# Optimization experiments

Measured on AMD Instinct MI355X. Metric: run time of the kernel, lower is better.

Reference implementation:

```python
import jax, jax.numpy as jnp
import numpy as np

EPS_LN = 1e-5
EPS_BN = 1e-5


def ln_channels(x, w, b):
    # LayerNorm2d: normalize over channel dim of NCHW
    mu = x.mean(axis=1, keepdims=True)
    var = x.var(axis=1, keepdims=True)
    return (x - mu) / jnp.sqrt(var + EPS_LN) * w[None, :, None, None] + b[None, :, None, None]


def bn_eval(x, g, b):
    # eval-mode BatchNorm2d with running_mean=0, running_var=1
    return x / jnp.sqrt(1.0 + EPS_BN) * g[None, :, None, None] + b[None, :, None, None]


def conv1x1(x, w, b):
    return jnp.einsum('bchw,oc->bohw', x, w) + b[None, :, None, None]


def q_shift(x):
    # directional shift: 4 channel quarters shifted right/left/down/up by 1 px (zero pad)
    C = x.shape[1]
    q = C // 4
    return jnp.concatenate([
        jnp.pad(x[:, 0 * q:1 * q, :, :-1], ((0, 0), (0, 0), (0, 0), (1, 0))),
        jnp.pad(x[:, 1 * q:2 * q, :, 1:], ((0, 0), (0, 0), (0, 0), (0, 1))),
        jnp.pad(x[:, 2 * q:3 * q, :-1, :], ((0, 0), (0, 0), (1, 0), (0, 0))),
        jnp.pad(x[:, 3 * q:4 * q, 1:, :], ((0, 0), (0, 0), (0, 1), (0, 0))),
    ], axis=1)


def wkv_scan(k, v, w_neg, u):
    # numerically-stable RWKV WKV recurrence. k, v: [N, T, C]; w_neg (negative decay), u: [C]
    N, T, C = k.shape

    def step(carry, kv):
        a, b, p = carry
        kt, vt = kv
        q = jnp.maximum(p, u + kt)
        e1 = jnp.exp(p - q)
        e2 = jnp.exp(u + kt - q)
        out = (e1 * a + e2 * vt) / (e1 * b + e2)
        q2 = jnp.maximum(p + w_neg, kt)
        f1 = jnp.exp(p + w_neg - q2)
        f2 = jnp.exp(kt - q2)
        return (f1 * a + f2 * vt, f1 * b + f2, q2), out

    init = (jnp.zeros((N, C), k.dtype), jnp.zeros((N, C), k.dtype), jnp.full((N, C), -1e38, k.dtype))
    _, outs = jax.lax.scan(step, init, (jnp.swapaxes(k, 0, 1), jnp.swapaxes(v, 0, 1)))
    return jnp.swapaxes(outs, 0, 1)


def shape_guided_rwkv(x, mask, mix_k, mix_v, mix_r, Wk, Wv, Wr, Wo, decay, first, kn_w, kn_b):
    B, C, H, W = x.shape
    xs = q_shift(x)
    x_sh = mask * xs + (1.0 - mask) * x  # saliency-guided shift blend
    mk = mix_k[None, :, None, None]
    mv = mix_v[None, :, None, None]
    mr = mix_r[None, :, None, None]
    xk = x * mk + x_sh * (1.0 - mk)
    xv = x * mv + x_sh * (1.0 - mv)
    xr = x * mr + x_sh * (1.0 - mr)
    k = jnp.einsum('bchw,oc->bohw', xk, Wk)
    v = jnp.einsum('bchw,oc->bohw', xv, Wv)
    sr = jax.nn.sigmoid(jnp.einsum('bchw,oc->bohw', xr, Wr))
    w_neg = -jnp.exp(decay)
    # horizontal orientation: scan each row left->right
    kh = k.transpose(0, 2, 3, 1).reshape(B * H, W, C)
    vh = v.transpose(0, 2, 3, 1).reshape(B * H, W, C)
    wkv_h = wkv_scan(kh, vh, w_neg, first).reshape(B, H, W, C).transpose(0, 3, 1, 2)
    # vertical orientation: scan each column top->bottom
    kv_ = k.transpose(0, 3, 2, 1).reshape(B * W, H, C)
    vv_ = v.transpose(0, 3, 2, 1).reshape(B * W, H, C)
    wkv_v = wkv_scan(kv_, vv_, w_neg, first).reshape(B, W, H, C).transpose(0, 3, 2, 1)
    wkv = 0.5 * (wkv_h + wkv_v)
    wkv = ln_channels(wkv, kn_w, kn_b)  # key_norm=True
    out = jnp.einsum('bchw,oc->bohw', sr * wkv, Wo)
    return x + out


def channel_fusion(x, c1_w, c1_b, bn1_g, bn1_b, c2_w, c2_b, bn2_g, bn2_b, c3_w, c3_b, bn3_g, bn3_b):
    # grouped 3x3 conv (groups=2) -> GELU -> BN -> 1x1 expand -> GELU -> BN -> 1x1 reduce -> GELU -> BN
    y = jax.lax.conv_general_dilated(x, c1_w, (1, 1), 'SAME',
                                     dimension_numbers=('NCHW', 'OIHW', 'NCHW'),
                                     feature_group_count=2) + c1_b[None, :, None, None]
    y = bn_eval(jax.nn.gelu(y, approximate=False), bn1_g, bn1_b)
    y = bn_eval(jax.nn.gelu(conv1x1(y, c2_w, c2_b), approximate=False), bn2_g, bn2_b)
    y = bn_eval(jax.nn.gelu(conv1x1(y, c3_w, c3_b), approximate=False), bn3_g, bn3_b)
    return y


def patch_expand(x, up_w, up_b, s=2):
    B, C, H, W = x.shape
    y = conv1x1(x, up_w, up_b)  # [B, Cout*s*s, H, W]
    Cout = y.shape[1] // (s * s)
    y = y.reshape(B, Cout, s, s, H, W).transpose(0, 1, 4, 2, 5, 3).reshape(B, Cout, H * s, W * s)
    return y


def setup_inputs() -> dict:
    key = jax.random.key(0)
    B, C, Cs, Cout, H, W, s = 8, 256, 512, 128, 64, 64, 2
    ks = jax.random.split(key, 32)
    sc = C ** -0.5
    inp = {
        'x': jax.random.normal(ks[0], (B, C, H, W), jnp.float32),
        'skip': jax.random.normal(ks[1], (B, Cs, H, W), jnp.float32),
        'saliency_mask': jax.random.uniform(ks[2], (B, 1, H, W), jnp.float32),
        'ln1_w': jnp.ones((C,)), 'ln1_b': jnp.zeros((C,)),
        'ln2_w': jnp.ones((C,)), 'ln2_b': jnp.zeros((C,)),
        'mix_k': jax.random.uniform(ks[3], (C,)),
        'mix_v': jax.random.uniform(ks[4], (C,)),
        'mix_r': jax.random.uniform(ks[5], (C,)),
        'Wk': jax.random.normal(ks[6], (C, C)) * sc,
        'Wv': jax.random.normal(ks[7], (C, C)) * sc,
        'Wr': jax.random.normal(ks[8], (C, C)) * sc,
        'Wo': jax.random.normal(ks[9], (C, C)) * sc,
        'decay': jax.random.normal(ks[10], (C,)) * 0.5,
        'first': jax.random.normal(ks[11], (C,)) * 0.5,
        'kn_w': jnp.ones((C,)), 'kn_b': jnp.zeros((C,)),
        'sp_w': jax.random.normal(ks[12], (C, Cs)) * (Cs ** -0.5),
        'sp_b': jnp.zeros((C,)),
        'c1_w': jax.random.normal(ks[13], (2 * C, C, 3, 3)) * ((C * 9) ** -0.5),
        'c1_b': jnp.zeros((2 * C,)),
        'bn1_g': jnp.ones((2 * C,)), 'bn1_b': jnp.zeros((2 * C,)),
        'c2_w': jax.random.normal(ks[14], (4 * C, 2 * C)) * ((2 * C) ** -0.5),
        'c2_b': jnp.zeros((4 * C,)),
        'bn2_g': jnp.ones((4 * C,)), 'bn2_b': jnp.zeros((4 * C,)),
        'c3_w': jax.random.normal(ks[15], (C, 4 * C)) * ((4 * C) ** -0.5),
        'c3_b': jnp.zeros((C,)),
        'bn3_g': jnp.ones((C,)), 'bn3_b': jnp.zeros((C,)),
        'up_w': jax.random.normal(ks[16], (Cout * s * s, C)) * sc,
        'up_b': jnp.zeros((Cout * s * s,)),
    }
    return inp


def reference(x, skip, saliency_mask, ln1_w, ln1_b, ln2_w, ln2_b, mix_k, mix_v, mix_r,
              Wk, Wv, Wr, Wo, decay, first, kn_w, kn_b, sp_w, sp_b,
              c1_w, c1_b, bn1_g, bn1_b, c2_w, c2_b, bn2_g, bn2_b, c3_w, c3_b, bn3_g, bn3_b,
              up_w, up_b):
    xn = ln_channels(x, ln1_w, ln1_b)
    x_sg = shape_guided_rwkv(xn, saliency_mask, mix_k, mix_v, mix_r, Wk, Wv, Wr, Wo,
                             decay, first, kn_w, kn_b)
    skip_feat = conv1x1(skip, sp_w, sp_b)
    x_cat = jnp.concatenate([x_sg, skip_feat], axis=1)
    x_fused = channel_fusion(x_cat, c1_w, c1_b, bn1_g, bn1_b, c2_w, c2_b, bn2_g, bn2_b,
                             c3_w, c3_b, bn3_g, bn3_b)
    x_fused = ln_channels(x_fused, ln2_w, ln2_b)
    return patch_expand(x_fused, up_w, up_b, s=2)
```

## Files before the change

### kernel.cpp

```cpp
#include <hip/hip_runtime.h>
#include <hip/hip_bf16.h>
#include <math.h>

#define B_ 8
#define C_ 256
#define P_ 4096

typedef __bf16 bf16_t;
typedef __attribute__((ext_vector_type(8))) __bf16 bf16x8;
typedef __attribute__((ext_vector_type(4))) float f32x4;

template<typename T>
__global__ __launch_bounds__(256)
void ln_stats_kernel(const T* __restrict__ in, float2* __restrict__ stats)
{
    __shared__ float sred[4][64];
    __shared__ float s2red[4][64];
    int tid = threadIdx.x;
    int wp = tid & 63, cw = tid >> 6;
    int gp = blockIdx.x * 64 + wp;
    int b  = gp >> 12, p = gp & 4095;
    size_t base = (size_t)b * 256 * 4096 + p;
    float s = 0.f, s2 = 0.f;
    #pragma unroll 8
    for (int cc = 0; cc < 64; ++cc) {
        float v = (float)in[base + (size_t)(cw * 64 + cc) * 4096];
        s += v; s2 += v * v;
    }
    sred[cw][wp] = s; s2red[cw][wp] = s2;
    __syncthreads();
    if (cw == 0) {
        s  = sred[0][wp]  + sred[1][wp]  + sred[2][wp]  + sred[3][wp];
        s2 = s2red[0][wp] + s2red[1][wp] + s2red[2][wp] + s2red[3][wp];
        float mu  = s * (1.f / 256.f);
        float var = s2 * (1.f / 256.f) - mu * mu;
        stats[gp] = make_float2(mu, 1.0f / sqrtf(var + 1e-5f));
    }
}

__global__ __launch_bounds__(256)
void qshift_mix_kernel(const float* __restrict__ x, const float2* __restrict__ st1,
                       const float* __restrict__ mask,
                       const float* __restrict__ gw, const float* __restrict__ gb,
                       const float* __restrict__ mk_, const float* __restrict__ mv_,
                       const float* __restrict__ mr_,
                       bf16_t* __restrict__ xk, bf16_t* __restrict__ xv,
                       bf16_t* __restrict__ xr)
{
    int g = blockIdx.x * 256 + threadIdx.x;
    int p = g & 4095;
    int c = (g >> 12) & 255;
    int b = g >> 20;
    int h = p >> 6, w = p & 63;
    float gwc = gw[c], gbc = gb[c];
    float2 stc = st1[(b << 12) + p];
    float xcv = (x[g] - stc.x) * stc.y * gwc + gbc;
    float xs = 0.f;
    int quad = c >> 6;
    int d = 0; bool ok = false;
    if (quad == 0)      { ok = (w > 0);  d = -1;  }
    else if (quad == 1) { ok = (w < 63); d = 1;   }
    else if (quad == 2) { ok = (h > 0);  d = -64; }
    else                { ok = (h < 63); d = 64;  }
    if (ok) {
        float2 st2 = st1[(b << 12) + p + d];
        xs = (x[g + d] - st2.x) * st2.y * gwc + gbc;
    }
    float m = mask[(b << 12) + p];
    float xsh = m * xs + (1.f - m) * xcv;
    float a;
    a = mk_[c]; xk[g] = (bf16_t)(a * xcv + (1.f - a) * xsh);
    a = mv_[c]; xv[g] = (bf16_t)(a * xcv + (1.f - a) * xsh);
    a = mr_[c]; xr[g] = (bf16_t)(a * xcv + (1.f - a) * xsh);
}

#define EP_NONE    0
#define EP_SIGMOID 1
#define EP_BIAS    2
#define EP_RESLN   3
#define EP_GELU_BN 4
#define EP_SHUFFLE 5
#define EP_KVR     6

template<int NB, int BMODE, int EPI, int OUTBF>
__global__ __launch_bounds__(256, 2)
void mfma_gemm(const bf16_t* __restrict__ Wp, const void* __restrict__ Xin,
               const bf16_t* __restrict__ X2,
               const float2* __restrict__ bstats, const float* __restrict__ blnw,
               const float* __restrict__ blnb,
               const float* __restrict__ bias, const float* __restrict__ bng,
               const float* __restrict__ bnb,
               const float* __restrict__ resx, const float2* __restrict__ estats,
               const float* __restrict__ elnw, const float* __restrict__ elnb,
               void* __restrict__ OutV,
               int O, int K, int Cstride, int obs, int ocoff)
{
    constexpr int BROWS = (NB == 3) ? 2 * 66 : 128;
    __shared__ bf16_t Alds[NB * 128 * 36];
    __shared__ bf16_t Blds[BROWS * 36];
    int tid = threadIdx.x;
    int bx = blockIdx.x;
    int o0 = blockIdx.y * 128;
    int b  = blockIdx.z;
    int p0 = bx << 7;
    int cbase = (NB == 3) ? ((o0 >> 8) << 8) : 0;

    const bf16_t* Wpe = (EPI == EP_KVR) ? Wp + (size_t)(b >> 3) * O * K : Wp;

    int lane = tid & 63, wid = tid >> 6;
    int l15 = lane & 15;
    int lk8 = (lane >> 4) << 3;
    int mbase = (wid >> 1) << 6;
    int nbase = (wid & 1) << 6;

    const bf16_t* Xb_bf = (const bf16_t*)Xin + (size_t)b * Cstride * 4096;
    const float*  Xb_f  = (const float*)Xin + (size_t)b * Cstride * 4096;
    const bf16_t* X2b   = (BMODE == 3) ? X2 + (size_t)b * Cstride * 4096 : nullptr;

    f32x4 acc[4][4] = {};

    if (NB == 3 && tid < 144) {
        int r = tid / 72, rest = tid % 72;
        int col = rest / 36, cc = rest % 36;
        Blds[(r * 66 + (col ? 65 : 0)) * 36 + cc] = (bf16_t)0.f;
    }

    for (int kh = 0; kh < NB; ++kh) {
        for (int c0 = 0; c0 < K; c0 += 32) {
            __syncthreads();
            if (NB == 3) {
                int wpos = tid & 63, cgr = tid >> 6;
                #pragma unroll
                for (int r = 0; r < 2; ++r) {
                    int hr = (bx << 1) + kh - 1 + r;
                    bf16x8 bv;
                    #pragma unroll
                    for (int i = 0; i < 8; ++i) bv[i] = (bf16_t)0.f;
                    if (hr >= 0 && hr < 64) {
                        size_t gb = (size_t)(cbase + c0 + cgr * 8) * 4096 + (hr << 6) + wpos;
                        #pragma unroll
                        for (int j = 0; j < 8; ++j) bv[j] = Xb_bf[gb + (size_t)j * 4096];
                    }
                    *reinterpret_cast<bf16x8*>(&Blds[(r * 66 + wpos + 1) * 36 + cgr * 8]) = bv;
                }
            } else {
                #pragma unroll
                for (int rep = 0; rep < 2; ++rep) {
                    int p_loc = tid & 127;
                    int cgr = (tid >> 7) + rep * 2;
                    bf16x8 bv;
                    size_t gbase = (size_t)(c0 + cgr * 8) * 4096 + p0 + p_loc;
                    float2 st = make_float2(0.f, 1.f);
                    if (BMODE >= 2) st = bstats[(b << 12) + p0 + p_loc];
                    #pragma unroll
                    for (int j = 0; j < 8; ++j) {
                        size_t gi = gbase + (size_t)j * 4096;
                        int cc = c0 + cgr * 8 + j;
                        if (BMODE == 0)      bv[j] = Xb_bf[gi];
                        else if (BMODE == 1) bv[j] = (bf16_t)Xb_f[gi];
                        else {
                            float v = ((float)Xb_bf[gi] - st.x) * st.y * blnw[cc] + blnb[cc];
                            if (BMODE == 3) v *= (float)X2b[gi];
                            bv[j] = (bf16_t)v;
                        }
                    }
                    *reinterpret_cast<bf16x8*>(&Blds[p_loc * 36 + cgr * 8]) = bv;
                }
            }
            {
                int ao = tid >> 1, aq = tid & 1;
                #pragma unroll
                for (int t = 0; t < NB; ++t) {
                    const bf16_t* wsrc = (NB == 3)
                        ? Wpe + ((size_t)(kh * 3 + t) * O + o0 + ao) * 256 + c0
                        : Wpe + (size_t)(o0 + ao) * K + c0;
                    bf16x8 w0 = *reinterpret_cast<const bf16x8*>(wsrc + aq * 8);
                    bf16x8 w1 = *reinterpret_cast<const bf16x8*>(wsrc + (aq + 2) * 8);
                    *reinterpret_cast<bf16x8*>(&Alds[(t * 128 + ao) * 36 + aq * 8]) = w0;
                    *reinterpret_cast<bf16x8*>(&Alds[(t * 128 + ao) * 36 + (aq + 2) * 8]) = w1;
                }
            }
            __syncthreads();
            #pragma unroll
            for (int t = 0; t < NB; ++t) {
                bf16x8 af[4];
                #pragma unroll
                for (int i = 0; i < 4; ++i)
                    af[i] = *reinterpret_cast<const bf16x8*>(
                              &Alds[(t * 128 + mbase + i * 16 + l15) * 36 + lk8]);
                #pragma unroll
                for (int j = 0; j < 4; ++j) {
                    int pl = nbase + j * 16;
                    int baddr;
                    if (NB == 3)
                        baddr = ((pl >> 6) * 66 + (pl & 63) + l15 + t) * 36 + lk8;
                    else
                        baddr = (pl + l15) * 36 + lk8;
                    bf16x8 bfv = *reinterpret_cast<const bf16x8*>(&Blds[baddr]);
                    #pragma unroll
                    for (int i = 0; i < 4; ++i)
                        acc[i][j] = __builtin_amdgcn_mfma_f32_16x16x32_bf16(
                                        af[i], bfv, acc[i][j], 0, 0, 0);
                }
            }
        }
    }

    const float bnsc = 1.0f / sqrtf(1.f + 1e-5f);
    bool kvr_sig = (EPI == EP_KVR) && (b >= 16);
    #pragma unroll
    for (int i = 0; i < 4; ++i) {
        #pragma unroll
        for (int r = 0; r < 4; ++r) {
            int o = o0 + mbase + i * 16 + ((lane >> 4) << 2) + r;
            float bi = (EPI == EP_BIAS || EPI == EP_GELU_BN || EPI == EP_SHUFFLE)
                       ? bias[o] : 0.f;
            float sc = 0.f, sh = 0.f;
            if (EPI == EP_GELU_BN) { sc = bng[o] * bnsc; sh = bnb[o]; }
            float rw = 0.f, rb = 0.f;
            if (EPI == EP_RESLN) { rw = elnw[o]; rb = elnb[o]; }
            #pragma unroll
            for (int j = 0; j < 4; ++j) {
                int pp = p0 + nbase + j * 16 + l15;
                float t = acc[i][j][r];
                if (EPI == EP_SIGMOID) t = 1.f / (1.f + expf(-t));
                if (EPI == EP_KVR && kvr_sig) t = 1.f / (1.f + expf(-t));
                if (EPI == EP_BIAS || EPI == EP_GELU_BN || EPI == EP_SHUFFLE) t += bi;
                if (EPI == EP_RESLN) {
                    float2 st = estats[(b << 12) + pp];
                    float rv = resx[((size_t)b * 256 + o) * 4096 + pp];
                    t += (rv - st.x) * st.y * rw + rb;
                }
                if (EPI == EP_GELU_BN) {
                    t = 0.5f * t * (1.f + erff(t * 0.70710678118654752f));
                    t = t * sc + sh;
                }
                if (EPI == EP_SHUFFLE) {
                    int co = o >> 2, s1 = (o >> 1) & 1, s2 = o & 1;
                    int hh = pp >> 6, ww = pp & 63;
                    ((float*)OutV)[(((size_t)b * 128 + co) * 128 + hh * 2 + s1) * 128
                                   + ww * 2 + s2] = t;
                } else {
                    size_t oidx = ((size_t)b * obs + ocoff + o) * 4096 + pp;
                    if (OUTBF) ((bf16_t*)OutV)[oidx] = (bf16_t)t;
                    else       ((float*)OutV)[oidx]  = t;
                }
            }
        }
    }
}

__global__ __launch_bounds__(256)
void pack_all_kernel(const float* __restrict__ wk, const float* __restrict__ wv,
                     const float* __restrict__ wr, const float* __restrict__ wo,
                     const float* __restrict__ sp, const float* __restrict__ c2,
                     const float* __restrict__ c3, const float* __restrict__ up,
                     const float* __restrict__ c1, bf16_t* __restrict__ outfl,
                     bf16_t* __restrict__ outc1)
{
    int g = blockIdx.x * 256 + threadIdx.x;
    if (g < 1310720) {
        float v;
        if      (g < 65536)   v = wk[g];
        else if (g < 131072)  v = wv[g - 65536];
        else if (g < 196608)  v = wr[g - 131072];
        else if (g < 262144)  v = wo[g - 196608];
        else if (g < 393216)  v = sp[g - 262144];
        else if (g < 917504)  v = c2[g - 393216];
        else if (g < 1179648) v = c3[g - 917504];
        else                  v = up[g - 1179648];
        outfl[g] = (bf16_t)v;
    } else {
        int g2 = g - 1310720;
        if (g2 < 1179648) {
            int c = g2 & 255;
            int o = (g2 >> 8) & 511;
            int tap = g2 >> 17;
            outc1[g2] = (bf16_t)c1[(size_t)o * 2304 + c * 9 + tap];
        }
    }
}

__global__ __launch_bounds__(64)
void wkv_h_kernel(const bf16_t* __restrict__ kin, const bf16_t* __restrict__ vin,
                  bf16_t* __restrict__ outw,
                  const float* __restrict__ decay, const float* __restrict__ first)
{
    __shared__ bf16_t ks[64 * 66];
    __shared__ bf16_t vs[64 * 66];
    int c0 = blockIdx.x * 64;
    int h  = blockIdx.y;
    int b  = blockIdx.z;
    int tid = threadIdx.x;
    size_t base = (((size_t)b * 256 + c0) * 64 + h) * 64;

    for (int f = tid; f < 64 * 64; f += 64) {
        int cc = f >> 6, w = f & 63;
        ks[cc * 66 + w] = kin[base + (size_t)cc * 4096 + w];
        vs[cc * 66 + w] = vin[base + (size_t)cc * 4096 + w];
    }
    __syncthreads();

    int c = c0 + tid;
    float u  = first[c];
    float wn = -expf(decay[c]);
    float a = 0.f, bb = 0.f, pp = -1e38f;
    for (int t = 0; t < 64; ++t) {
        float kt = (float)ks[tid * 66 + t], vt = (float)vs[tid * 66 + t];
        float q  = fmaxf(pp, u + kt);
        float e1 = expf(pp - q), e2 = expf(u + kt - q);
        float ov = (e1 * a + e2 * vt) / (e1 * bb + e2);
        ks[tid * 66 + t] = (bf16_t)ov;
        float q2 = fmaxf(pp + wn, kt);
        float f1 = expf(pp + wn - q2), f2 = expf(kt - q2);
        a = f1 * a + f2 * vt;
        bb = f1 * bb + f2;
        pp = q2;
    }
    __syncthreads();
    for (int f = tid; f < 64 * 64; f += 64) {
        int cc = f >> 6, w = f & 63;
        outw[base + (size_t)cc * 4096 + w] = ks[cc * 66 + w];
    }
}

__global__ __launch_bounds__(256)
void wkv_v_kernel(const bf16_t* __restrict__ kin, const bf16_t* __restrict__ vin,
                  bf16_t* __restrict__ outw,
                  const float* __restrict__ decay, const float* __restrict__ first)
{
    int g = blockIdx.x * 256 + threadIdx.x;
    int w = g & 63;
    int c = (g >> 6) & 255;
    int b = g >> 14;
    size_t base = (size_t)(b * 256 + c) * 4096 + w;
    float u  = first[c];
    float wn = -expf(decay[c]);
    float a = 0.f, bb = 0.f, pp = -1e38f;
    for (int h = 0; h < 64; ++h) {
        size_t idx = base + h * 64;
        float kt = (float)kin[idx], vt = (float)vin[idx];
        float q  = fmaxf(pp, u + kt);
        float e1 = expf(pp - q), e2 = expf(u + kt - q);
        float ov = (e1 * a + e2 * vt) / (e1 * bb + e2);
        outw[idx] = (bf16_t)(0.5f * ((float)outw[idx] + ov));
        float q2 = fmaxf(pp + wn, kt);
        float f1 = expf(pp + wn - q2), f2 = expf(kt - q2);
        a = f1 * a + f2 * vt;
        bb = f1 * bb + f2;
        pp = q2;
    }
}

extern "C" void kernel_launch(void* const* d_in, const int* in_sizes, int n_in,
                              void* d_out, int out_size, void* d_ws, size_t ws_size,
                              hipStream_t stream)
{
    const float* x      = (const float*)d_in[0];
    const float* skip   = (const float*)d_in[1];
    const float* mask   = (const float*)d_in[2];
    const float* ln1_w  = (const float*)d_in[3];
    const float* ln1_b  = (const float*)d_in[4];
    const float* ln2_w  = (const float*)d_in[5];
    const float* ln2_b  = (const float*)d_in[6];
    const float* mix_k  = (const float*)d_in[7];
    const float* mix_v  = (const float*)d_in[8];
    const float* mix_r  = (const float*)d_in[9];
    const float* Wk     = (const float*)d_in[10];
    const float* Wv     = (const float*)d_in[11];
    const float* Wr     = (const float*)d_in[12];
    const float* Wo     = (const float*)d_in[13];
    const float* decay  = (const float*)d_in[14];
    const float* first  = (const float*)d_in[15];
    const float* kn_w   = (const float*)d_in[16];
    const float* kn_b   = (const float*)d_in[17];
    const float* sp_w   = (const float*)d_in[18];
    const float* sp_b   = (const float*)d_in[19];
    const float* c1_w   = (const float*)d_in[20];
    const float* c1_b   = (const float*)d_in[21];
    const float* bn1_g  = (const float*)d_in[22];
    const float* bn1_b  = (const float*)d_in[23];
    const float* c2_w   = (const float*)d_in[24];
    const float* c2_b   = (const float*)d_in[25];
    const float* bn2_g  = (const float*)d_in[26];
    const float* bn2_b  = (const float*)d_in[27];
    const float* c3_w   = (const float*)d_in[28];
    const float* c3_b   = (const float*)d_in[29];
    const float* bn3_g  = (const float*)d_in[30];
    const float* bn3_b  = (const float*)d_in[31];
    const float* up_w   = (const float*)d_in[32];
    const float* up_b   = (const float*)d_in[33];
    float* out = (float*)d_out;

    float* ws = (float*)d_ws;
    const size_t S = 8388608;
    const size_t Hs = S / 2;
    bf16_t* xk   = (bf16_t*)ws;
    bf16_t* xv   = (bf16_t*)(ws + Hs);
    bf16_t* xr   = (bf16_t*)(ws + 2 * Hs);
    bf16_t* kbuf = (bf16_t*)(ws + 3 * Hs);
    bf16_t* vbuf = (bf16_t*)(ws + 4 * Hs);
    bf16_t* rbuf = (bf16_t*)(ws + 5 * Hs);
    bf16_t* wkv  = (bf16_t*)(ws + 6 * Hs);
    bf16_t* xcat = (bf16_t*)(ws + 7 * Hs);
    bf16_t* y1   = (bf16_t*)(ws + 9 * Hs);
    bf16_t* y2   = (bf16_t*)ws;
    bf16_t* y3   = (bf16_t*)(ws + 4 * Hs);
    float*  wtop = ws + 11 * Hs;
    bf16_t* w9   = (bf16_t*)wtop;
    bf16_t* wfl  = w9 + 1179648;
    float2* st1  = (float2*)(wfl + 1310720);
    float2* stk  = st1 + 32768;
    float2* st2  = stk + 32768;
    bf16_t* wkb = wfl;
    bf16_t* wob = wfl + 196608;
    bf16_t* spb = wfl + 262144;
    bf16_t* c2b = wfl + 393216;
    bf16_t* c3b = wfl + 917504;
    bf16_t* upb = wfl + 1179648;

    dim3 blk(256);

    pack_all_kernel<<<dim3(9728), blk, 0, stream>>>(Wk, Wv, Wr, Wo, sp_w, c2_w,
                                                    c3_w, up_w, c1_w, wfl, w9);
    ln_stats_kernel<float><<<dim3(512), blk, 0, stream>>>(x, st1);

    qshift_mix_kernel<<<dim3(32768), blk, 0, stream>>>(x, st1, mask, ln1_w, ln1_b,
                                                       mix_k, mix_v, mix_r, xk, xv, xr);
    mfma_gemm<1, 0, EP_KVR, 1><<<dim3(32, 2, 24), blk, 0, stream>>>(
        wkb, xk, nullptr, nullptr, nullptr, nullptr, nullptr, nullptr, nullptr,
        nullptr, nullptr, nullptr, nullptr, kbuf, 256, 256, 256, 256, 0);
    wkv_h_kernel<<<dim3(4, 64, 8), dim3(64), 0, stream>>>(kbuf, vbuf, wkv, decay, first);
    wkv_v_kernel<<<dim3(512), blk, 0, stream>>>(kbuf, vbuf, wkv, decay, first);
    ln_stats_kernel<bf16_t><<<dim3(512), blk, 0, stream>>>(wkv, stk);
    mfma_gemm<1, 3, EP_RESLN, 1><<<dim3(32, 2, 8), blk, 0, stream>>>(
        wob, wkv, rbuf, stk, kn_w, kn_b, nullptr, nullptr, nullptr,
        x, st1, ln1_w, ln1_b, xcat, 256, 256, 256, 512, 0);
    mfma_gemm<1, 1, EP_BIAS, 1><<<dim3(32, 2, 8), blk, 0, stream>>>(
        spb, skip, nullptr, nullptr, nullptr, nullptr, sp_b, nullptr, nullptr,
        nullptr, nullptr, nullptr, nullptr, xcat, 256, 512, 512, 512, 256);
    mfma_gemm<3, 0, EP_GELU_BN, 1><<<dim3(32, 4, 8), blk, 0, stream>>>(
        w9, xcat, nullptr, nullptr, nullptr, nullptr, c1_b, bn1_g, bn1_b,
        nullptr, nullptr, nullptr, nullptr, y1, 512, 256, 512, 512, 0);
    mfma_gemm<1, 0, EP_GELU_BN, 1><<<dim3(32, 8, 8), blk, 0, stream>>>(
        c2b, y1, nullptr, nullptr, nullptr, nullptr, c2_b, bn2_g, bn2_b,
        nullptr, nullptr, nullptr, nullptr, y2, 1024, 512, 512, 1024, 0);
    mfma_gemm<1, 0, EP_GELU_BN, 1><<<dim3(32, 2, 8), blk, 0, stream>>>(
        c3b, y2, nullptr, nullptr, nullptr, nullptr, c3_b, bn3_g, bn3_b,
        nullptr, nullptr, nullptr, nullptr, y3, 256, 1024, 1024, 256, 0);
    ln_stats_kernel<bf16_t><<<dim3(512), blk, 0, stream>>>(y3, st2);
    mfma_gemm<1, 2, EP_SHUFFLE, 0><<<dim3(32, 4, 8), blk, 0, stream>>>(
        upb, y3, nullptr, st2, ln2_w, ln2_b, up_b, nullptr, nullptr,
        nullptr, nullptr, nullptr, nullptr, out, 512, 256, 256, 0, 0);
}
```

Measured before the change: 531.0 us.

## Load GEMM weight tiles directly into LDS with swizzled layout

Replaces the register-staged weight tile copy in the MFMA GEMM with global_load_lds direct-to-LDS transfers into an unpadded 32-wide row layout. To avoid LDS bank conflicts without padding, weights are pre-swizzled during packing with an XOR pattern on 8-element column groups, and the fragment reads apply the matching swizzle. This saves VGPR traffic and LDS footprint, but it couples the pack kernel layout to the GEMM read pattern and depends on the swizzle being consistent for every weight matrix.

```diff
diff --git a/kernel.cpp b/kernel.cpp
--- a/kernel.cpp
+++ b/kernel.cpp
@@ -9,6 +9,12 @@
 typedef __bf16 bf16_t;
 typedef __attribute__((ext_vector_type(8))) __bf16 bf16x8;
 typedef __attribute__((ext_vector_type(4))) float f32x4;
+
+__device__ __forceinline__ int swzc(int o, int c)
+{
+    int f = (o & 3) ^ ((o >> 2) & 3);
+    return (c & ~31) | ((((c >> 3) & 3) ^ f) << 3) | (c & 7);
+}
 
 template<typename T>
 __global__ __launch_bounds__(256)
@@ -96,7 +102,7 @@
                int O, int K, int Cstride, int obs, int ocoff)
 {
     constexpr int BROWS = (NB == 3) ? 2 * 66 : 128;
-    __shared__ bf16_t Alds[NB * 128 * 36];
+    __shared__ bf16_t Alds[NB * 128 * 32];
     __shared__ bf16_t Blds[BROWS * 36];
     int tid = threadIdx.x;
     int bx = blockIdx.x;
@@ -109,9 +115,11 @@
 
     int lane = tid & 63, wid = tid >> 6;
     int l15 = lane & 15;
-    int lk8 = (lane >> 4) << 3;
     int mbase = (wid >> 1) << 6;
     int nbase = (wid & 1) << 6;
+    int fsw = (l15 & 3) ^ ((l15 >> 2) & 3);
+    int aoff8 = (((lane >> 4) ^ fsw) << 3);
+    int lk8 = (lane >> 4) << 3;
 
     const bf16_t* Xb_bf = (const bf16_t*)Xin + (size_t)b * Cstride * 4096;
     const float*  Xb_f  = (const float*)Xin + (size_t)b * Cstride * 4096;
@@ -167,17 +175,19 @@
                     *reinterpret_cast<bf16x8*>(&Blds[p_loc * 36 + cgr * 8]) = bv;
                 }
             }
-            {
-                int ao = tid >> 1, aq = tid & 1;
+            #pragma unroll
+            for (int t = 0; t < NB; ++t) {
                 #pragma unroll
-                for (int t = 0; t < NB; ++t) {
-                    const bf16_t* wsrc = (NB == 3)
-                        ? Wpe + ((size_t)(kh * 3 + t) * O + o0 + ao) * 256 + c0
-                        : Wpe + (size_t)(o0 + ao) * K + c0;
-                    bf16x8 w0 = *reinterpret_cast<const bf16x8*>(wsrc + aq * 8);
-                    bf16x8 w1 = *reinterpret_cast<const bf16x8*>(wsrc + (aq + 2) * 8);
-                    *reinterpret_cast<bf16x8*>(&Alds[(t * 128 + ao) * 36 + aq * 8]) = w0;
-                    *reinterpret_cast<bf16x8*>(&Alds[(t * 128 + ao) * 36 + (aq + 2) * 8]) = w1;
+                for (int q = 0; q < 2; ++q) {
+                    int r0 = (wid * 2 + q) * 16;
+                    int row = o0 + r0 + (lane >> 2);
+                    const bf16_t* gaddr = (NB == 3)
+                        ? Wpe + ((size_t)(kh * 3 + t) * O + row) * 256 + c0 + ((lane & 3) << 3)
+                        : Wpe + (size_t)row * K + c0 + ((lane & 3) << 3);
+                    bf16_t* laddr = Alds + t * 4096 + (wid * 2 + q) * 512;
+                    __builtin_amdgcn_global_load_lds(
+                        (const __attribute__((address_space(1))) void*)gaddr,
+                        (__attribute__((address_space(3))) void*)laddr, 16, 0, 0);
                 }
             }
             __syncthreads();
@@ -187,7 +197,7 @@
                 #pragma unroll
                 for (int i = 0; i < 4; ++i)
                     af[i] = *reinterpret_cast<const bf16x8*>(
-                              &Alds[(t * 128 + mbase + i * 16 + l15) * 36 + lk8]);
+                              &Alds[(t * 128 + mbase + i * 16 + l15) * 32 + aoff8]);
                 #pragma unroll
                 for (int j = 0; j < 4; ++j) {
                     int pl = nbase + j * 16;
@@ -260,23 +270,26 @@
 {
     int g = blockIdx.x * 256 + threadIdx.x;
     if (g < 1310720) {
-        float v;
-        if      (g < 65536)   v = wk[g];
-        else if (g < 131072)  v = wv[g - 65536];
-        else if (g < 196608)  v = wr[g - 131072];
-        else if (g < 262144)  v = wo[g - 196608];
-        else if (g < 393216)  v = sp[g - 262144];
-        else if (g < 917504)  v = c2[g - 393216];
-        else if (g < 1179648) v = c3[g - 917504];
-        else                  v = up[g - 1179648];
-        outfl[g] = (bf16_t)v;
+        const float* src; int base, ksh;
+        if      (g < 65536)   { src = wk; base = 0;       ksh = 8;  }
+        else if (g < 131072)  { src = wv; base = 65536;   ksh = 8;  }
+        else if (g < 196608)  { src = wr; base = 131072;  ksh = 8;  }
+        else if (g < 262144)  { src = wo; base = 196608;  ksh = 8;  }
+        else if (g < 393216)  { src = sp; base = 262144;  ksh = 9;  }
+        else if (g < 917504)  { src = c2; base = 393216;  ksh = 9;  }
+        else if (g < 1179648) { src = c3; base = 917504;  ksh = 10; }
+        else                  { src = up; base = 1179648; ksh = 8;  }
+        int local = g - base;
+        int o = local >> ksh;
+        int c = local & ((1 << ksh) - 1);
+        outfl[g] = (bf16_t)src[((size_t)o << ksh) + swzc(o, c)];
     } else {
         int g2 = g - 1310720;
         if (g2 < 1179648) {
             int c = g2 & 255;
             int o = (g2 >> 8) & 511;
             int tap = g2 >> 17;
-            outc1[g2] = (bf16_t)c1[(size_t)o * 2304 + c * 9 + tap];
+            outc1[g2] = (bf16_t)c1[(size_t)o * 2304 + swzc(o, c) * 9 + tap];
         }
     }
 }
```

Result: slower. 545.0 us (+2.6%).
